# Kernel optimization log

Hardware: AMD Instinct MI355X
Metric: run time of the kernel (lower is better)

Reference implementation:

```python
import jax, jax.numpy as jnp
import numpy as np

ALPHA = 4.0  # spikingjelly default Sigmoid surrogate alpha
BN_EPS = 1e-5

@jax.custom_vjp
def _spike(v):
    return (v >= 0.0).astype(v.dtype)

def _spike_fwd(v):
    return _spike(v), v

def _spike_bwd(v, g):
    s = jax.nn.sigmoid(ALPHA * v)
    return (g * ALPHA * s * (1.0 - s),)

_spike.defvjp(_spike_fwd, _spike_bwd)

def lif(x, v_th):
    # Single-step LIFNode(tau=2, v_reset=0) starting from v=0:
    # v = v + (x - v)/tau = x/2 ; spike = Heaviside(v - v_th)
    return _spike(x * 0.5 - v_th)

def bn(x, p):
    # p: [4, C] = gamma, beta, running_mean, running_var (inference BN)
    g, b, m, v = p
    scale = g * jax.lax.rsqrt(v + BN_EPS)
    return x * scale[None, :, None, None] + (b - m * scale)[None, :, None, None]

def conv1x1(x, w):
    # x: [B,C,H,W], w: [O,C]
    return jnp.einsum('bchw,oc->bohw', x, w)

def dwconv3x3(x, w):
    # depthwise 3x3, w: [C,3,3]
    C = x.shape[1]
    return jax.lax.conv_general_dilated(
        x, w[:, None], (1, 1), 'SAME',
        feature_group_count=C,
        dimension_numbers=('NCHW', 'OIHW', 'NCHW'))

def branch(x, w1, dw, w2, bns):
    # RepConv: conv1x1 -> BN -> (dw3x3 -> pw1x1 -> BN), then the extra Sequential BN
    x = bn(conv1x1(x, w1), bns[0])
    x = bn(conv1x1(dwconv3x3(x, dw), w2), bns[1])
    return bn(x, bns[2])

def setup_inputs() -> dict:
    key = jax.random.key(0)
    ks = jax.random.split(key, 5)
    B, C, H, W = 16, 256, 80, 80
    x = jax.random.normal(ks[0], (B, C, H, W), jnp.float32) * 2.0  # so LIFs actually fire
    w1 = jax.random.normal(ks[1], (4, C, C), jnp.float32) * 0.06
    dw = jax.random.normal(ks[2], (4, C, 3, 3), jnp.float32) * 0.3
    w2 = jax.random.normal(ks[3], (4, C, C), jnp.float32) * 0.06
    bn_params = jax.random.uniform(ks[4], (4, 3, 4, C), jnp.float32, 0.1, 1.0)
    return {"x": x, "w1": w1, "dw": dw, "w2": w2, "bn_params": bn_params}

def reference(x, w1, dw, w2, bn_params):
    scale = 0.125
    xs = lif(x, 1.0)                                   # head_lif
    q = branch(xs, w1[0], dw[0], w2[0], bn_params[0])  # q_conv (q_lif unused in source)
    k = branch(xs, w1[1], dw[1], w2[1], bn_params[1])  # k_conv (k_lif unused in source)
    v = branch(xs, w1[2], dw[2], w2[2], bn_params[2])  # v_conv
    v = lif(v, 1.0)                                    # v_lif -> binary spikes
    # k.transpose(-2,-1) @ v : per (b,c) [W,H] @ [H,W] -> [W,W]
    kv = jnp.einsum('bchw,bchu->bcwu', k, v)
    # q @ kv : [H,W] @ [W,W] -> [H,W]
    attn = jnp.einsum('bchw,bcwu->bchu', q, kv) * scale
    s = lif(attn, 0.5)                                 # attn_lif, v_threshold=0.5
    return branch(s, w1[3], dw[3], w2[3], bn_params[3])  # proj_conv
```

## Files before the change

### kernel.cpp

```cpp
#include <hip/hip_runtime.h>
#include <hip/hip_bf16.h>
#include <cstdint>
#include <cstddef>
#include <cmath>

typedef unsigned short u16;
typedef unsigned char  u8;
typedef unsigned int   u32;
typedef __attribute__((ext_vector_type(8))) short short8;
typedef __attribute__((ext_vector_type(4))) float f32x4;
typedef __attribute__((ext_vector_type(4))) u16 u16x4;

#define CCH 256
#define HWP 6400

__device__ __forceinline__ u16 f2bf(float f) {
  u32 u = __float_as_uint(f);
  u = (u + 0x7FFFu + ((u >> 16) & 1u)) >> 16;
  return (u16)u;
}
__device__ __forceinline__ float bf2f(u16 h) { return __uint_as_float(((u32)h) << 16); }
__device__ __forceinline__ void split3(float v, u16& h, u16& m, u16& l) {
  h = f2bf(v); float r = v - bf2f(h);
  m = f2bf(r); l = f2bf(r - bf2f(m));
}
__device__ __forceinline__ void gl_lds16(const void* g, void* l) {
  __builtin_amdgcn_global_load_lds((const __attribute__((address_space(1))) unsigned int*)g,
                                   (__attribute__((address_space(3))) unsigned int*)l,
                                   16, 0, 0);
}

__global__ __launch_bounds__(256) void fold_weights(
    const float* __restrict__ w1, const float* __restrict__ w2,
    const float* __restrict__ bnp,
    u16* __restrict__ w1h, u16* __restrict__ w1m, u16* __restrict__ w1l,
    u16* __restrict__ w2h, u16* __restrict__ w2m, u16* __restrict__ w2l,
    float* __restrict__ b0f, float* __restrict__ b2f)
{
  int i = blockIdx.x >> 8, o = blockIdx.x & 255, c = threadIdx.x;
  const float* bp = bnp + i * 3072;
  double g0 = bp[0 + o],    be0 = bp[256 + o],  m0 = bp[512 + o],  v0 = bp[768 + o];
  double g1 = bp[1024 + o], be1 = bp[1280 + o], m1 = bp[1536 + o], v1 = bp[1792 + o];
  double g2 = bp[2048 + o], be2 = bp[2304 + o], m2 = bp[2560 + o], v2 = bp[2816 + o];
  double s0 = g0 / sqrt(v0 + 1e-5);
  double s1 = g1 / sqrt(v1 + 1e-5);
  double s2 = g2 / sqrt(v2 + 1e-5);
  size_t ro = (size_t)(i * 256 + o) * 256;
  float wa = (float)(s0 * (double)w1[ro + c]);
  float wb = (float)(s1 * s2 * (double)w2[ro + c]);
  u16 h, m, l;
  split3(wa, h, m, l); w1h[ro + c] = h; w1m[ro + c] = m; w1l[ro + c] = l;
  split3(wb, h, m, l); w2h[ro + c] = h; w2m[ro + c] = m; w2l[ro + c] = l;
  if (c == 0) {
    b0f[i * 256 + o] = (float)(be0 - m0 * s0);
    b2f[i * 256 + o] = (float)(s2 * (be1 - m1 * s1) + be2 - m2 * s2);
  }
}

__global__ __launch_bounds__(256) void head_spike(
    const float* __restrict__ x, u8* __restrict__ xs, int b0)
{
  __shared__ u8 tile[64][68];
  int z = blockIdx.z, c0 = blockIdx.y << 6, p0 = blockIdx.x << 6;
  int tid = threadIdx.x;
  const float* xb = x + ((size_t)(b0 + z) * CCH + c0) * HWP + p0;
#pragma unroll
  for (int j = 0; j < 16; ++j) {
    int idx = j * 256 + tid;
    int cl = idx >> 6, pl = idx & 63;
    tile[pl][cl] = (xb[(size_t)cl * HWP + pl] >= 2.0f) ? 1 : 0;
  }
  __syncthreads();
#pragma unroll
  for (int j = 0; j < 4; ++j) {
    int idx = j * 256 + tid;
    int row = idx >> 4, c4 = (idx & 15) << 2;
    *(uchar4*)(xs + ((size_t)z * HWP + p0 + row) * CCH + c0 + c4) =
        *(const uchar4*)&tile[row][c4];
  }
}

__global__ __launch_bounds__(256) void transpose_s(
    const u8* __restrict__ in, u8* __restrict__ out, int b0)
{
  __shared__ u8 tile[64][68];
  int z = blockIdx.z, c0 = blockIdx.y << 6, p0 = blockIdx.x << 6;
  int tid = threadIdx.x;
#pragma unroll
  for (int j = 0; j < 4; ++j) {
    int idx = j * 256 + tid;
    int cl = idx >> 4, p4 = (idx & 15) << 2;
    uchar4 v = *(const uchar4*)(in + ((size_t)z * CCH + c0 + cl) * HWP + p0 + p4);
    tile[p4 + 0][cl] = v.x; tile[p4 + 1][cl] = v.y;
    tile[p4 + 2][cl] = v.z; tile[p4 + 3][cl] = v.w;
  }
  __syncthreads();
#pragma unroll
  for (int j = 0; j < 4; ++j) {
    int idx = j * 256 + tid;
    int row = idx >> 4, c4 = (idx & 15) << 2;
    *(uchar4*)(out + ((size_t)(b0 + z) * HWP + p0 + row) * CCH + c0 + c4) =
        *(const uchar4*)&tile[row][c4];
  }
}

__global__ __launch_bounds__(256) void gemm1(
    const u8* __restrict__ act, int b0in,
    const u16* __restrict__ WH, const u16* __restrict__ WM, const u16* __restrict__ WL,
    const float* __restrict__ bias, float* __restrict__ T1)
{
  __shared__ alignas(16) u16 As[128 * 40];
  __shared__ alignas(16) u16 LWH[4096];
  __shared__ alignas(16) u16 LWM[4096];
  __shared__ alignas(16) u16 LWL[4096];
  const int tid = threadIdx.x, wave = tid >> 6, lane = tid & 63;
  const int p0 = blockIdx.x * 128, o0 = blockIdx.y * 128, z = blockIdx.z;
  const int wm = (wave >> 1) * 64, wn = (wave & 1) * 64;
  const int lc = lane & 15, lr = lane >> 4;
  const u8* ab = act + ((size_t)(b0in + z) * HWP + p0) * CCH;
  const char* whb = (const char*)(WH + (size_t)o0 * 256);
  const char* wmb = (const char*)(WM + (size_t)o0 * 256);
  const char* wlb = (const char*)(WL + (size_t)o0 * 256);

  f32x4 acc[4][4];
#pragma unroll
  for (int i = 0; i < 4; ++i)
#pragma unroll
    for (int j = 0; j < 4; ++j) acc[i][j] = (f32x4){0.f, 0.f, 0.f, 0.f};

  const int srow = tid >> 1, shalf = tid & 1;

  for (int kc = 0; kc < 8; ++kc) {
    const int kof = kc * 64;
    __syncthreads();
#pragma unroll
    for (int t = 0; t < 2; ++t) {
      int li = t * 256 + tid;
      int row = li >> 2, ch = li & 3;
      int chp = (ch - row - (row >> 2)) & 3;
      size_t so = (size_t)row * 512 + kof + chp * 16;
      int base = (t * 256 + wave * 64) * 8;
      gl_lds16(whb + so, &LWH[base]);
      gl_lds16(wmb + so, &LWM[base]);
      gl_lds16(wlb + so, &LWL[base]);
    }
    uint4 u = *(const uint4*)(ab + (size_t)srow * CCH + kc * 32 + shalf * 16);
    u32 vv[4] = {u.x, u.y, u.z, u.w};
    u32 w[8];
#pragma unroll
    for (int q = 0; q < 4; ++q) {
      u32 v = vv[q];
      w[2 * q]     = ((v & 255u) ? 0x3F80u : 0u) | (((v >> 8) & 255u) ? 0x3F800000u : 0u);
      w[2 * q + 1] = (((v >> 16) & 255u) ? 0x3F80u : 0u) | (((v >> 24) & 255u) ? 0x3F800000u : 0u);
    }
    *(uint4*)&As[srow * 40 + shalf * 16]     = (uint4){w[0], w[1], w[2], w[3]};
    *(uint4*)&As[srow * 40 + shalf * 16 + 8] = (uint4){w[4], w[5], w[6], w[7]};
    __syncthreads();
    short8 af[4];
#pragma unroll
    for (int i = 0; i < 4; ++i)
      af[i] = *(const short8*)&As[(wm + i * 16 + lc) * 40 + lr * 8];
#pragma unroll
    for (int j = 0; j < 4; ++j) {
      int row = wn + j * 16 + lc;
      int o = row * 32 + ((lr + lc + (lc >> 2)) & 3) * 8;
      short8 bh = *(const short8*)&LWH[o];
      short8 bm = *(const short8*)&LWM[o];
      short8 bl = *(const short8*)&LWL[o];
#pragma unroll
      for (int i = 0; i < 4; ++i) {
        acc[i][j] = __builtin_amdgcn_mfma_f32_16x16x32_bf16(af[i], bl, acc[i][j], 0, 0, 0);
        acc[i][j] = __builtin_amdgcn_mfma_f32_16x16x32_bf16(af[i], bm, acc[i][j], 0, 0, 0);
        acc[i][j] = __builtin_amdgcn_mfma_f32_16x16x32_bf16(af[i], bh, acc[i][j], 0, 0, 0);
      }
    }
  }
  float* tb = T1 + ((size_t)z * HWP + p0) * CCH + o0;
#pragma unroll
  for (int j = 0; j < 4; ++j) {
    int n = wn + j * 16 + lc;
    float bn_ = bias[o0 + n];
#pragma unroll
    for (int i = 0; i < 4; ++i) {
      int m = wm + i * 16 + lr * 4;
#pragma unroll
      for (int r = 0; r < 4; ++r)
        tb[(size_t)(m + r) * CCH + n] = acc[i][j][r] + bn_;
    }
  }
}

__global__ __launch_bounds__(256) void dw3(
    const float* __restrict__ t1, const float* __restrict__ dwk,
    u16* __restrict__ oh, u16* __restrict__ om, u16* __restrict__ ol)
{
  __shared__ float wl[2304];
  int tid = threadIdx.x;
#pragma unroll
  for (int t = 0; t < 9; ++t) wl[t * 256 + tid] = dwk[t * 256 + tid];
  int c4 = (tid & 63) << 2;
  int pl = tid >> 6;
  int p = blockIdx.x * 4 + pl;
  int z = blockIdx.y;
  int y = p / 80, x = p - y * 80;
  __syncthreads();
  float a0 = 0.f, a1 = 0.f, a2 = 0.f, a3 = 0.f;
  const float* base = t1 + (size_t)z * HWP * CCH;
  const float* wc = &wl[c4 * 9];
#pragma unroll
  for (int dy = -1; dy <= 1; ++dy) {
    int yy = y + dy;
    bool vy = (unsigned)yy < 80u;
#pragma unroll
    for (int dx = -1; dx <= 1; ++dx) {
      int xx = x + dx;
      if (vy && (unsigned)xx < 80u) {
        float4 v = *(const float4*)(base + (size_t)(yy * 80 + xx) * CCH + c4);
        int t = (dy + 1) * 3 + (dx + 1);
        a0 += wc[t]      * v.x;
        a1 += wc[9 + t]  * v.y;
        a2 += wc[18 + t] * v.z;
        a3 += wc[27 + t] * v.w;
      }
    }
  }
  u16 h0, m0, l0, h1, m1, l1, h2, m2, l2, h3, m3, l3;
  split3(a0, h0, m0, l0);
  split3(a1, h1, m1, l1);
  split3(a2, h2, m2, l2);
  split3(a3, h3, m3, l3);
  u16x4 vh, vm, vlo;
  vh.x = h0; vh.y = h1; vh.z = h2; vh.w = h3;
  vm.x = m0; vm.y = m1; vm.z = m2; vm.w = m3;
  vlo.x = l0; vlo.y = l1; vlo.z = l2; vlo.w = l3;
  size_t addr = ((size_t)z * HWP + p) * CCH + c4;
  *(u16x4*)(oh + addr) = vh;
  *(u16x4*)(om + addr) = vm;
  *(u16x4*)(ol + addr) = vlo;
}

template <int MODE>
__global__ __launch_bounds__(256) void gemm2s(
    const u16* __restrict__ AH, const u16* __restrict__ AM, const u16* __restrict__ AL,
    const u16* __restrict__ WH, const u16* __restrict__ WM, const u16* __restrict__ WL,
    const float* __restrict__ bias, int b0,
    float* __restrict__ outF, u8* __restrict__ outB,
    u16* __restrict__ outH, u16* __restrict__ outM, u16* __restrict__ outL)
{
  __shared__ alignas(16) u16 LAH[4096];
  __shared__ alignas(16) u16 LAM[4096];
  __shared__ alignas(16) u16 LAL[4096];
  __shared__ alignas(16) u16 LWH[4096];
  __shared__ alignas(16) u16 LWM[4096];
  __shared__ alignas(16) u16 LWL[4096];
  const int tid = threadIdx.x, wave = tid >> 6, lane = tid & 63;
  const int p0 = blockIdx.x * 128, o0 = blockIdx.y * 128, z = blockIdx.z;
  const int wm = (wave >> 1) * 64, wn = (wave & 1) * 64;
  const int lc = lane & 15, lr = lane >> 4;
  const char* ahb = (const char*)(AH + ((size_t)z * HWP + p0) * 256);
  const char* amb = (const char*)(AM + ((size_t)z * HWP + p0) * 256);
  const char* alb = (const char*)(AL + ((size_t)z * HWP + p0) * 256);
  const char* whb = (const char*)(WH + (size_t)o0 * 256);
  const char* wmb = (const char*)(WM + (size_t)o0 * 256);
  const char* wlb = (const char*)(WL + (size_t)o0 * 256);

  f32x4 acc[4][4];
#pragma unroll
  for (int i = 0; i < 4; ++i)
#pragma unroll
    for (int j = 0; j < 4; ++j) acc[i][j] = (f32x4){0.f, 0.f, 0.f, 0.f};

  for (int kc = 0; kc < 8; ++kc) {
    const int kof = kc * 64;
#pragma unroll
    for (int t = 0; t < 2; ++t) {
      int li = t * 256 + tid;
      int row = li >> 2, ch = li & 3;
      int chp = (ch - row - (row >> 2)) & 3;
      size_t so = (size_t)row * 512 + kof + chp * 16;
      int base = (t * 256 + wave * 64) * 8;
      gl_lds16(ahb + so, &LAH[base]);
      gl_lds16(amb + so, &LAM[base]);
      gl_lds16(alb + so, &LAL[base]);
      gl_lds16(whb + so, &LWH[base]);
      gl_lds16(wmb + so, &LWM[base]);
      gl_lds16(wlb + so, &LWL[base]);
    }
    __syncthreads();
    short8 afH[4], afM[4], afL[4];
#pragma unroll
    for (int i = 0; i < 4; ++i) {
      int row = wm + i * 16 + lc;
      int o = row * 32 + ((lr + lc + (lc >> 2)) & 3) * 8;
      afH[i] = *(const short8*)&LAH[o];
      afM[i] = *(const short8*)&LAM[o];
      afL[i] = *(const short8*)&LAL[o];
    }
#pragma unroll
    for (int j = 0; j < 4; ++j) {
      int row = wn + j * 16 + lc;
      int o = row * 32 + ((lr + lc + (lc >> 2)) & 3) * 8;
      short8 bh = *(const short8*)&LWH[o];
      short8 bm = *(const short8*)&LWM[o];
      short8 bl = *(const short8*)&LWL[o];
#pragma unroll
      for (int i = 0; i < 4; ++i) {
        acc[i][j] = __builtin_amdgcn_mfma_f32_16x16x32_bf16(afM[i], bm, acc[i][j], 0, 0, 0);
        acc[i][j] = __builtin_amdgcn_mfma_f32_16x16x32_bf16(afL[i], bh, acc[i][j], 0, 0, 0);
        acc[i][j] = __builtin_amdgcn_mfma_f32_16x16x32_bf16(afH[i], bl, acc[i][j], 0, 0, 0);
        acc[i][j] = __builtin_amdgcn_mfma_f32_16x16x32_bf16(afM[i], bh, acc[i][j], 0, 0, 0);
        acc[i][j] = __builtin_amdgcn_mfma_f32_16x16x32_bf16(afH[i], bm, acc[i][j], 0, 0, 0);
        acc[i][j] = __builtin_amdgcn_mfma_f32_16x16x32_bf16(afH[i], bh, acc[i][j], 0, 0, 0);
      }
    }
    __syncthreads();
  }
#pragma unroll
  for (int j = 0; j < 4; ++j) {
    int n = o0 + wn + j * 16 + lc;
    float bn_ = bias[n];
    size_t rowb = ((size_t)(b0 + z) * CCH + n) * HWP + p0;
#pragma unroll
    for (int i = 0; i < 4; ++i) {
      int m = wm + i * 16 + lr * 4;
      if (MODE == 0) {
        float4 o;
        o.x = acc[i][j][0] + bn_; o.y = acc[i][j][1] + bn_;
        o.z = acc[i][j][2] + bn_; o.w = acc[i][j][3] + bn_;
        *(float4*)(outF + rowb + m) = o;
      } else if (MODE == 1) {
        uchar4 o;
        o.x = (acc[i][j][0] + bn_ >= 2.0f) ? 1 : 0;
        o.y = (acc[i][j][1] + bn_ >= 2.0f) ? 1 : 0;
        o.z = (acc[i][j][2] + bn_ >= 2.0f) ? 1 : 0;
        o.w = (acc[i][j][3] + bn_ >= 2.0f) ? 1 : 0;
        *(uchar4*)(outB + rowb + m) = o;
      } else {
        u16x4 vh, vm2, vl2;
#pragma unroll
        for (int r = 0; r < 4; ++r) {
          u16 hh, mm, ll;
          split3(acc[i][j][r] + bn_, hh, mm, ll);
          vh[r] = hh; vm2[r] = mm; vl2[r] = ll;
        }
        *(u16x4*)(outH + rowb + m) = vh;
        *(u16x4*)(outM + rowb + m) = vm2;
        *(u16x4*)(outL + rowb + m) = vl2;
      }
    }
  }
}

__global__ __launch_bounds__(320) void attn_k(
    const u16* __restrict__ qh_g, const u16* __restrict__ qm_g, const u16* __restrict__ ql_g,
    const u16* __restrict__ kh_g, const u16* __restrict__ km_g, const u16* __restrict__ kl_g,
    const u8* __restrict__ vv, u8* __restrict__ s)
{
  __shared__ alignas(16) u16 L[24960];
  __shared__ alignas(16) u8  VT[8320];
  const int tid = threadIdx.x, wave = tid >> 6, lane = tid & 63;
  const int lc = lane & 15, lr = lane >> 4;
  const size_t off = (size_t)blockIdx.x * HWP;
  u16* KH = L; u16* KM = L + 8320; u16* KL = L + 16640;

  short8 qfr[3][3];
  const int hrow = wave * 16 + lc;
#pragma unroll
  for (int kc = 0; kc < 3; ++kc) {
    int w0 = kc * 32 + lr * 8;
    if (w0 < 80) {
      size_t qo = off + (size_t)hrow * 80 + w0;
      qfr[kc][0] = *(const short8*)(qh_g + qo);
      qfr[kc][1] = *(const short8*)(qm_g + qo);
      qfr[kc][2] = *(const short8*)(ql_g + qo);
    } else {
      qfr[kc][0] = (short8){0, 0, 0, 0, 0, 0, 0, 0};
      qfr[kc][1] = qfr[kc][0];
      qfr[kc][2] = qfr[kc][0];
    }
  }

#pragma unroll
  for (int t = 0; t < 3; ++t) {
    int g = t * 320 + tid;
    int h = g / 12, wc = g - h * 12;
    int dst = h * 104 + wc * 8;
    if (wc < 10) {
      size_t so = off + (size_t)h * 80 + wc * 8;
      *(short8*)&KH[dst] = *(const short8*)(kh_g + so);
      *(short8*)&KM[dst] = *(const short8*)(km_g + so);
      *(short8*)&KL[dst] = *(const short8*)(kl_g + so);
    } else {
      short8 z8 = (short8){0, 0, 0, 0, 0, 0, 0, 0};
      *(short8*)&KH[dst] = z8; *(short8*)&KM[dst] = z8; *(short8*)&KL[dst] = z8;
    }
  }
  {
    int row = tid >> 2, qq = tid & 3;
    *(u32*)&VT[row * 104 + 80 + qq * 4] = 0;
  }
#pragma unroll
  for (int t = 0; t < 5; ++t) {
    int q = t * 320 + tid;
    int h = q / 20, w4 = (q - h * 20) * 4;
    uchar4 v4 = *(const uchar4*)(vv + off + (size_t)h * 80 + w4);
    VT[(w4 + 0) * 104 + h] = v4.x;
    VT[(w4 + 1) * 104 + h] = v4.y;
    VT[(w4 + 2) * 104 + h] = v4.z;
    VT[(w4 + 3) * 104 + h] = v4.w;
  }
  __syncthreads();

  f32x4 accS[5];
#pragma unroll
  for (int n = 0; n < 5; ++n) accS[n] = (f32x4){0.f, 0.f, 0.f, 0.f};
  for (int kc = 0; kc < 3; ++kc) {
#pragma unroll
    for (int n = 0; n < 5; ++n) {
      int bo = (n * 16 + lc) * 104 + kc * 32 + lr * 8;
      short8 kh_ = *(const short8*)&KH[bo];
      short8 km_ = *(const short8*)&KM[bo];
      short8 kl_ = *(const short8*)&KL[bo];
      __builtin_amdgcn_s_setprio(1);
      accS[n] = __builtin_amdgcn_mfma_f32_16x16x32_bf16(qfr[kc][0], kl_, accS[n], 0, 0, 0);
      accS[n] = __builtin_amdgcn_mfma_f32_16x16x32_bf16(qfr[kc][2], kh_, accS[n], 0, 0, 0);
      accS[n] = __builtin_amdgcn_mfma_f32_16x16x32_bf16(qfr[kc][1], km_, accS[n], 0, 0, 0);
      accS[n] = __builtin_amdgcn_mfma_f32_16x16x32_bf16(qfr[kc][1], kh_, accS[n], 0, 0, 0);
      accS[n] = __builtin_amdgcn_mfma_f32_16x16x32_bf16(qfr[kc][0], km_, accS[n], 0, 0, 0);
      accS[n] = __builtin_amdgcn_mfma_f32_16x16x32_bf16(qfr[kc][0], kh_, accS[n], 0, 0, 0);
      __builtin_amdgcn_s_setprio(0);
    }
  }
  __syncthreads();
#pragma unroll
  for (int n = 0; n < 5; ++n) {
#pragma unroll
    for (int r = 0; r < 4; ++r) {
      u16 hh, mm, ll; split3(accS[n][r], hh, mm, ll);
      int o = (wave * 16 + lr * 4 + r) * 104 + n * 16 + lc;
      KH[o] = hh; KM[o] = mm; KL[o] = ll;
    }
  }
  __syncthreads();
  f32x4 accA[5];
#pragma unroll
  for (int n = 0; n < 5; ++n) accA[n] = (f32x4){0.f, 0.f, 0.f, 0.f};
  for (int kc = 0; kc < 3; ++kc) {
    int ao = (wave * 16 + lc) * 104 + kc * 32 + lr * 8;
    short8 sh_ = *(const short8*)&KH[ao];
    short8 sm_ = *(const short8*)&KM[ao];
    short8 sl_ = *(const short8*)&KL[ao];
#pragma unroll
    for (int n = 0; n < 5; ++n) {
      const u8* vp = &VT[(n * 16 + lc) * 104 + kc * 32 + lr * 8];
      u32 b0 = *(const u32*)vp;
      u32 b1 = *(const u32*)(vp + 4);
      u32 e0 = ((b0 & 255u) ? 0x3F80u : 0u) | (((b0 >> 8) & 255u) ? 0x3F800000u : 0u);
      u32 e1 = (((b0 >> 16) & 255u) ? 0x3F80u : 0u) | (((b0 >> 24) & 255u) ? 0x3F800000u : 0u);
      u32 e2 = ((b1 & 255u) ? 0x3F80u : 0u) | (((b1 >> 8) & 255u) ? 0x3F800000u : 0u);
      u32 e3 = (((b1 >> 16) & 255u) ? 0x3F80u : 0u) | (((b1 >> 24) & 255u) ? 0x3F800000u : 0u);
      u32 vbw[4] = {e0, e1, e2, e3};
      short8 vb = *(const short8*)vbw;
      __builtin_amdgcn_s_setprio(1);
      accA[n] = __builtin_amdgcn_mfma_f32_16x16x32_bf16(sl_, vb, accA[n], 0, 0, 0);
      accA[n] = __builtin_amdgcn_mfma_f32_16x16x32_bf16(sm_, vb, accA[n], 0, 0, 0);
      accA[n] = __builtin_amdgcn_mfma_f32_16x16x32_bf16(sh_, vb, accA[n], 0, 0, 0);
      __builtin_amdgcn_s_setprio(0);
    }
  }
#pragma unroll
  for (int n = 0; n < 5; ++n)
#pragma unroll
    for (int r = 0; r < 4; ++r)
      s[off + (size_t)(wave * 16 + lr * 4 + r) * 80 + n * 16 + lc] =
          (accA[n][r] >= 8.0f) ? 1 : 0;
}

extern "C" void kernel_launch(void* const* d_in, const int* in_sizes, int n_in,
                              void* d_out, int out_size, void* d_ws, size_t ws_size,
                              hipStream_t stream)
{
  const float* x   = (const float*)d_in[0];
  const float* w1  = (const float*)d_in[1];
  const float* dwk = (const float*)d_in[2];
  const float* w2  = (const float*)d_in[3];
  const float* bnp = (const float*)d_in[4];
  float* out = (float*)d_out;
  char* ws = (char*)d_ws;

  u16* W1H = (u16*)(ws + 0);
  u16* W1M = (u16*)(ws + 524288);
  u16* W1L = (u16*)(ws + 1048576);
  u16* W2H = (u16*)(ws + 1572864);
  u16* W2M = (u16*)(ws + 2097152);
  u16* W2L = (u16*)(ws + 2621440);
  float* B0F = (float*)(ws + 3145728);
  float* B2F = (float*)(ws + 3149824);
  u8*    SPM = (u8*)(ws + 3153920);
  u8*    XS  = (u8*)(ws + 29368320);
  float* T1  = (float*)(ws + 42475520);
  u16*   KH_ = (u16*)(ws + 42475520);
  u16*   KM_ = (u16*)(ws + 68689920);
  u16*   QH_ = (u16*)(ws + 94904320);
  u16*   QM_ = (u16*)(ws + 121118720);
  u16*   QL_ = (u16*)(ws + 147333120);
  u16*   KL_ = (u16*)(ws + 173547520);
  u8*    V   = (u8*)(ws + 199761920);
  u16*   D2H = (u16*)(ws + 212869120);
  u16*   D2M = (u16*)(ws + 239083520);
  u16*   D2L = (u16*)(ws + 265297920);

  dim3 gb(256);
  fold_weights<<<dim3(1024), gb, 0, stream>>>(w1, w2, bnp,
      W1H, W1M, W1L, W2H, W2M, W2L, B0F, B2F);

  for (int c = 0; c < 2; ++c) {
    int b0 = c * 8;
    dim3 gh(100, 4, 8), gg(50, 2, 8), gd(1600, 8);
    head_spike<<<gh, gb, 0, stream>>>(x, XS, b0);
    gemm1<<<gg, gb, 0, stream>>>(XS, 0, W1H + 2 * 65536, W1M + 2 * 65536, W1L + 2 * 65536,
                                 B0F + 512, T1);
    dw3<<<gd, gb, 0, stream>>>(T1, dwk + 2 * 2304, D2H, D2M, D2L);
    gemm2s<1><<<gg, gb, 0, stream>>>(D2H, D2M, D2L,
                                     W2H + 2 * 65536, W2M + 2 * 65536, W2L + 2 * 65536,
                                     B2F + 512, 0, nullptr, V, nullptr, nullptr, nullptr);
    gemm1<<<gg, gb, 0, stream>>>(XS, 0, W1H + 0 * 65536, W1M + 0 * 65536, W1L + 0 * 65536,
                                 B0F + 0, T1);
    dw3<<<gd, gb, 0, stream>>>(T1, dwk + 0 * 2304, D2H, D2M, D2L);
    gemm2s<2><<<gg, gb, 0, stream>>>(D2H, D2M, D2L,
                                     W2H + 0 * 65536, W2M + 0 * 65536, W2L + 0 * 65536,
                                     B2F + 0, 0, nullptr, nullptr, QH_, QM_, QL_);
    gemm1<<<gg, gb, 0, stream>>>(XS, 0, W1H + 1 * 65536, W1M + 1 * 65536, W1L + 1 * 65536,
                                 B0F + 256, T1);
    dw3<<<gd, gb, 0, stream>>>(T1, dwk + 1 * 2304, D2H, D2M, D2L);
    gemm2s<2><<<gg, gb, 0, stream>>>(D2H, D2M, D2L,
                                     W2H + 1 * 65536, W2M + 1 * 65536, W2L + 1 * 65536,
                                     B2F + 256, 0, nullptr, nullptr, KH_, KM_, KL_);
    attn_k<<<dim3(2048), dim3(320), 0, stream>>>(QH_, QM_, QL_, KH_, KM_, KL_, V, V);
    transpose_s<<<gh, gb, 0, stream>>>(V, SPM, b0);
  }
  for (int c = 0; c < 2; ++c) {
    int b0 = c * 8;
    dim3 gg(50, 2, 8), gd(1600, 8);
    gemm1<<<gg, gb, 0, stream>>>(SPM, b0, W1H + 3 * 65536, W1M + 3 * 65536, W1L + 3 * 65536,
                                 B0F + 768, T1);
    dw3<<<gd, gb, 0, stream>>>(T1, dwk + 3 * 2304, D2H, D2M, D2L);
    gemm2s<0><<<gg, gb, 0, stream>>>(D2H, D2M, D2L,
                                     W2H + 3 * 65536, W2M + 3 * 65536, W2L + 3 * 65536,
                                     B2F + 768, b0, out, nullptr, nullptr, nullptr, nullptr);
  }
}
```

Measured before the change: 1.438 ms.

## Load gemm2s A fragments directly from global and raise occupancy bounds

In gemm2s the A operand (three bf16 split planes) is no longer staged through LDS. Each wave loads its MFMA A fragments straight from global memory in two halves, which cuts LDS use in half and lowers register pressure. Both gemm kernels also get a launch_bounds minimum of 4 blocks per CU. The aim is higher occupancy and less LDS traffic. In exchange, A fragments are read redundantly from global/L2 by the two waves sharing rows, and the reads are no longer coalesced through LDS, which could raise memory latency.

```diff
diff --git a/kernel.cpp b/kernel.cpp
--- a/kernel.cpp
+++ b/kernel.cpp
@@ -104,7 +104,7 @@
   }
 }
 
-__global__ __launch_bounds__(256) void gemm1(
+__global__ __launch_bounds__(256, 4) void gemm1(
     const u8* __restrict__ act, int b0in,
     const u16* __restrict__ WH, const u16* __restrict__ WM, const u16* __restrict__ WL,
     const float* __restrict__ bias, float* __restrict__ T1)
@@ -240,16 +240,13 @@
 }
 
 template <int MODE>
-__global__ __launch_bounds__(256) void gemm2s(
+__global__ __launch_bounds__(256, 4) void gemm2s(
     const u16* __restrict__ AH, const u16* __restrict__ AM, const u16* __restrict__ AL,
     const u16* __restrict__ WH, const u16* __restrict__ WM, const u16* __restrict__ WL,
     const float* __restrict__ bias, int b0,
     float* __restrict__ outF, u8* __restrict__ outB,
     u16* __restrict__ outH, u16* __restrict__ outM, u16* __restrict__ outL)
 {
-  __shared__ alignas(16) u16 LAH[4096];
-  __shared__ alignas(16) u16 LAM[4096];
-  __shared__ alignas(16) u16 LAL[4096];
   __shared__ alignas(16) u16 LWH[4096];
   __shared__ alignas(16) u16 LWM[4096];
   __shared__ alignas(16) u16 LWL[4096];
@@ -257,9 +254,10 @@
   const int p0 = blockIdx.x * 128, o0 = blockIdx.y * 128, z = blockIdx.z;
   const int wm = (wave >> 1) * 64, wn = (wave & 1) * 64;
   const int lc = lane & 15, lr = lane >> 4;
-  const char* ahb = (const char*)(AH + ((size_t)z * HWP + p0) * 256);
-  const char* amb = (const char*)(AM + ((size_t)z * HWP + p0) * 256);
-  const char* alb = (const char*)(AL + ((size_t)z * HWP + p0) * 256);
+  const size_t abase = ((size_t)z * HWP + p0) * 256;
+  const u16* ah = AH + abase;
+  const u16* am = AM + abase;
+  const u16* al = AL + abase;
   const char* whb = (const char*)(WH + (size_t)o0 * 256);
   const char* wmb = (const char*)(WM + (size_t)o0 * 256);
   const char* wlb = (const char*)(WL + (size_t)o0 * 256);
@@ -270,8 +268,14 @@
 #pragma unroll
     for (int j = 0; j < 4; ++j) acc[i][j] = (f32x4){0.f, 0.f, 0.f, 0.f};
 
+  int aoff[4];
+#pragma unroll
+  for (int i = 0; i < 4; ++i) aoff[i] = (wm + i * 16 + lc) * 256 + lr * 8;
+
+#pragma unroll 1
   for (int kc = 0; kc < 8; ++kc) {
     const int kof = kc * 64;
+    const int ka  = kc * 32;
 #pragma unroll
     for (int t = 0; t < 2; ++t) {
       int li = t * 256 + tid;
@@ -279,23 +283,18 @@
       int chp = (ch - row - (row >> 2)) & 3;
       size_t so = (size_t)row * 512 + kof + chp * 16;
       int base = (t * 256 + wave * 64) * 8;
-      gl_lds16(ahb + so, &LAH[base]);
-      gl_lds16(amb + so, &LAM[base]);
-      gl_lds16(alb + so, &LAL[base]);
       gl_lds16(whb + so, &LWH[base]);
       gl_lds16(wmb + so, &LWM[base]);
       gl_lds16(wlb + so, &LWL[base]);
     }
+    short8 aH[2], aM[2], aL[2];
+#pragma unroll
+    for (int u = 0; u < 2; ++u) {
+      aH[u] = *(const short8*)(ah + aoff[u] + ka);
+      aM[u] = *(const short8*)(am + aoff[u] + ka);
+      aL[u] = *(const short8*)(al + aoff[u] + ka);
+    }
     __syncthreads();
-    short8 afH[4], afM[4], afL[4];
-#pragma unroll
-    for (int i = 0; i < 4; ++i) {
-      int row = wm + i * 16 + lc;
-      int o = row * 32 + ((lr + lc + (lc >> 2)) & 3) * 8;
-      afH[i] = *(const short8*)&LAH[o];
-      afM[i] = *(const short8*)&LAM[o];
-      afL[i] = *(const short8*)&LAL[o];
-    }
 #pragma unroll
     for (int j = 0; j < 4; ++j) {
       int row = wn + j * 16 + lc;
@@ -304,13 +303,36 @@
       short8 bm = *(const short8*)&LWM[o];
       short8 bl = *(const short8*)&LWL[o];
 #pragma unroll
-      for (int i = 0; i < 4; ++i) {
-        acc[i][j] = __builtin_amdgcn_mfma_f32_16x16x32_bf16(afM[i], bm, acc[i][j], 0, 0, 0);
-        acc[i][j] = __builtin_amdgcn_mfma_f32_16x16x32_bf16(afL[i], bh, acc[i][j], 0, 0, 0);
-        acc[i][j] = __builtin_amdgcn_mfma_f32_16x16x32_bf16(afH[i], bl, acc[i][j], 0, 0, 0);
-        acc[i][j] = __builtin_amdgcn_mfma_f32_16x16x32_bf16(afM[i], bh, acc[i][j], 0, 0, 0);
-        acc[i][j] = __builtin_amdgcn_mfma_f32_16x16x32_bf16(afH[i], bm, acc[i][j], 0, 0, 0);
-        acc[i][j] = __builtin_amdgcn_mfma_f32_16x16x32_bf16(afH[i], bh, acc[i][j], 0, 0, 0);
+      for (int u = 0; u < 2; ++u) {
+        acc[u][j] = __builtin_amdgcn_mfma_f32_16x16x32_bf16(aM[u], bm, acc[u][j], 0, 0, 0);
+        acc[u][j] = __builtin_amdgcn_mfma_f32_16x16x32_bf16(aL[u], bh, acc[u][j], 0, 0, 0);
+        acc[u][j] = __builtin_amdgcn_mfma_f32_16x16x32_bf16(aH[u], bl, acc[u][j], 0, 0, 0);
+        acc[u][j] = __builtin_amdgcn_mfma_f32_16x16x32_bf16(aM[u], bh, acc[u][j], 0, 0, 0);
+        acc[u][j] = __builtin_amdgcn_mfma_f32_16x16x32_bf16(aH[u], bm, acc[u][j], 0, 0, 0);
+        acc[u][j] = __builtin_amdgcn_mfma_f32_16x16x32_bf16(aH[u], bh, acc[u][j], 0, 0, 0);
+      }
+    }
+#pragma unroll
+    for (int u = 0; u < 2; ++u) {
+      aH[u] = *(const short8*)(ah + aoff[2 + u] + ka);
+      aM[u] = *(const short8*)(am + aoff[2 + u] + ka);
+      aL[u] = *(const short8*)(al + aoff[2 + u] + ka);
+    }
+#pragma unroll
+    for (int j = 0; j < 4; ++j) {
+      int row = wn + j * 16 + lc;
+      int o = row * 32 + ((lr + lc + (lc >> 2)) & 3) * 8;
+      short8 bh = *(const short8*)&LWH[o];
+      short8 bm = *(const short8*)&LWM[o];
+      short8 bl = *(const short8*)&LWL[o];
+#pragma unroll
+      for (int u = 0; u < 2; ++u) {
+        acc[2 + u][j] = __builtin_amdgcn_mfma_f32_16x16x32_bf16(aM[u], bm, acc[2 + u][j], 0, 0, 0);
+        acc[2 + u][j] = __builtin_amdgcn_mfma_f32_16x16x32_bf16(aL[u], bh, acc[2 + u][j], 0, 0, 0);
+        acc[2 + u][j] = __builtin_amdgcn_mfma_f32_16x16x32_bf16(aH[u], bl, acc[2 + u][j], 0, 0, 0);
+        acc[2 + u][j] = __builtin_amdgcn_mfma_f32_16x16x32_bf16(aM[u], bh, acc[2 + u][j], 0, 0, 0);
+        acc[2 + u][j] = __builtin_amdgcn_mfma_f32_16x16x32_bf16(aH[u], bm, acc[2 + u][j], 0, 0, 0);
+        acc[2 + u][j] = __builtin_amdgcn_mfma_f32_16x16x32_bf16(aH[u], bh, acc[2 + u][j], 0, 0, 0);
       }
     }
     __syncthreads();
```

New measurement: 2.042 ms. 1.42x slower.
